# Performance work log

Measured on AMD Instinct MI355X. Metric: run time of the kernel, lower is better.

Reference implementation:

```python
import jax, jax.numpy as jnp
import numpy as np

B, T, C, H, W = 1, 8, 128, 64, 64
F = 64  # num_feat


def setup_inputs() -> dict:
    key = jax.random.key(0)
    ks = jax.random.split(key, 8)
    return {
        "input1": jax.random.normal(ks[0], (B, T, C, H, W), jnp.float32),
        "input2": jax.random.normal(ks[1], (B, T, C, H, W), jnp.float32),
        "W1": jax.random.normal(ks[2], (F, C), jnp.float32) * 0.05,
        "b1": jax.random.normal(ks[3], (F,), jnp.float32) * 0.05,
        "W2": jax.random.normal(ks[4], (F, C), jnp.float32) * 0.05,
        "b2": jax.random.normal(ks[5], (F,), jnp.float32) * 0.05,
        "W3": jax.random.normal(ks[6], (F, C), jnp.float32) * 0.05,
        "b3": jax.random.normal(ks[7], (F,), jnp.float32) * 0.05,
    }


def reference(input1, input2, W1, b1, W2, b2, W3, b3):
    # act == 0 (ReLU branch). Conv1d(kernel=1) == per-position linear projection.
    b, t, c, h, w = input1.shape
    n = h * w
    x1 = input1.reshape(b, t, c, n)  # matches transpose(1,2).reshape then frame slice
    x2 = input2.reshape(b, t, c, n)
    q = jnp.einsum('fc,btcn->btnf', W1, x1) + b1          # [B,T,N,F]
    k = jnp.einsum('fc,btcn->btnf', W2, x2) + b2          # [B,T,N,F]
    g = jnp.einsum('fc,btcn->btnf', W3, x1) + b3          # [B,T,N,F]
    scores = jax.nn.relu(jnp.einsum('btnf,btmf->btnm', q, k))  # [B,T,N,N]
    out = jnp.einsum('btnm,btmf->btnf', scores, g)        # [B,T,N,F]
    # view([B,H,W,F]).permute(0,3,1,2), stacked over T -> [B,T,F,H,W]
    return out.reshape(b, t, h, w, -1).transpose(0, 1, 4, 2, 3)
```

## Files before the change

### kernel.cpp

```cpp
#include <hip/hip_runtime.h>
#include <hip/hip_bf16.h>

constexpr int T = 8;
constexpr int C = 128;
constexpr int N = 4096;
constexpr int F = 64;

typedef __bf16 bf16x8 __attribute__((ext_vector_type(8)));
typedef __bf16 bf16x4 __attribute__((ext_vector_type(4)));
typedef __bf16 bf16x2 __attribute__((ext_vector_type(2)));
typedef float  f32x4  __attribute__((ext_vector_type(4)));
typedef float  f32x16 __attribute__((ext_vector_type(16)));

__global__ __launch_bounds__(256) void setup_kernel(
    const float* __restrict__ W1, const float* __restrict__ W2,
    const float* __restrict__ W3, __bf16* __restrict__ Wb,
    float* __restrict__ out)
{
    int i = blockIdx.x * 256 + threadIdx.x;
    ((f32x4*)out)[i] = (f32x4){0.f, 0.f, 0.f, 0.f};
    if (i < 3 * F * C) {
        int p = i >> 13, r = i & 8191;
        const float* W = (p == 0) ? W1 : (p == 1) ? W2 : W3;
        Wb[i] = (__bf16)W[r];
    }
}

__global__ __launch_bounds__(256) void proj_kernel(
    const float* __restrict__ x1, const float* __restrict__ x2,
    const __bf16* __restrict__ Wb,
    const float* __restrict__ b1, const float* __restrict__ b2,
    const float* __restrict__ b3,
    __bf16* __restrict__ Qb, __bf16* __restrict__ Kb, __bf16* __restrict__ Gw)
{
    const int pj = blockIdx.y;
    const int t  = blockIdx.x >> 6;
    const int nb = blockIdx.x & 63;
    const int n0 = nb * 64;

    constexpr int XS = 136;
    __shared__ __bf16 Xt[64 * XS];

    const float* X = (pj == 1) ? x2 : x1;

    const int tid = threadIdx.x;
    const int ng  = tid & 15;
    const int cgi = tid >> 4;

#pragma unroll
    for (int pass = 0; pass < 2; ++pass) {
        const int c0 = cgi * 4 + pass * 64;
        const size_t base = ((size_t)t * C + c0) * (size_t)N + n0 + ng * 4;
        f32x4 v[4];
#pragma unroll
        for (int i = 0; i < 4; ++i)
            v[i] = *(const f32x4*)&X[base + (size_t)i * N];
#pragma unroll
        for (int j = 0; j < 4; ++j) {
            bf16x4 o;
#pragma unroll
            for (int i = 0; i < 4; ++i) o[i] = (__bf16)v[i][j];
            *(bf16x4*)&Xt[(ng * 4 + j) * XS + c0] = o;
        }
    }
    __syncthreads();

    const int wave = tid >> 6, lane = tid & 63;
    const int quad = lane >> 4, l16 = lane & 15;

    bf16x8 a[4];
#pragma unroll
    for (int cc = 0; cc < 4; ++cc)
        a[cc] = *(const bf16x8*)&Xt[(wave * 16 + l16) * XS + cc * 32 + quad * 8];

    const __bf16* W = Wb + (size_t)pj * F * C;

    if (pj < 2) {
        const float* bias = pj ? b2 : b1;
        __bf16*      O    = pj ? Kb : Qb;

        f32x4 acc[4];
#pragma unroll
        for (int ft = 0; ft < 4; ++ft) acc[ft] = (f32x4){0.f, 0.f, 0.f, 0.f};
#pragma unroll
        for (int cc = 0; cc < 4; ++cc) {
#pragma unroll
            for (int ft = 0; ft < 4; ++ft) {
                bf16x8 wf = *(const bf16x8*)&W[(ft * 16 + l16) * C + cc * 32 + quad * 8];
                acc[ft] = __builtin_amdgcn_mfma_f32_16x16x32_bf16(wf, a[cc], acc[ft], 0, 0, 0);
            }
        }
        const int n = n0 + wave * 16 + l16;
#pragma unroll
        for (int ft = 0; ft < 4; ++ft) {
            const int f0 = ft * 16 + quad * 4;
            f32x4 bv = *(const f32x4*)&bias[f0];
            bf16x4 o;
#pragma unroll
            for (int r = 0; r < 4; ++r) o[r] = (__bf16)(acc[ft][r] + bv[r]);
            *(bf16x4*)&O[((size_t)t * N + n) * F + f0] = o;
        }
    } else {
        f32x4 acc[4];
#pragma unroll
        for (int ft = 0; ft < 4; ++ft) acc[ft] = (f32x4){0.f, 0.f, 0.f, 0.f};
#pragma unroll
        for (int cc = 0; cc < 4; ++cc) {
#pragma unroll
            for (int ft = 0; ft < 4; ++ft) {
                bf16x8 wf = *(const bf16x8*)&W[(ft * 16 + l16) * C + cc * 32 + quad * 8];
                acc[ft] = __builtin_amdgcn_mfma_f32_16x16x32_bf16(a[cc], wf, acc[ft], 0, 0, 0);
            }
        }
        const int nr0 = n0 + wave * 16 + quad * 4;
#pragma unroll
        for (int ft = 0; ft < 4; ++ft) {
            const int f = ft * 16 + l16;
            const float bv = b3[f];
            bf16x4 o;
#pragma unroll
            for (int r = 0; r < 4; ++r) o[r] = (__bf16)(acc[ft][r] + bv);
            *(bf16x4*)&Gw[((size_t)t * F + f) * (size_t)N + nr0] = o;
        }
    }
}

constexpr int KSPLIT = 4;

__global__ __launch_bounds__(512, 4) void attn_kernel(
    const __bf16* __restrict__ Qb, const __bf16* __restrict__ Kb,
    const __bf16* __restrict__ Gw, float* __restrict__ out)
{
    const int ks = blockIdx.x & (KSPLIT - 1);
    const int qb = (blockIdx.x / KSPLIT) & 15;
    const int t  = blockIdx.x / (KSPLIT * 16);
    const int q0 = qb * 256;

    constexpr int KS = 72;
    __shared__ __bf16 Kt[64 * KS];
    __shared__ __bf16 Gt[64 * KS];

    const int tid = threadIdx.x, wave = tid >> 6, lane = tid & 63;
    const int m32 = lane & 31, hi = lane >> 5;

    bf16x8 qf[4];
    {
        const __bf16* qrow = &Qb[((size_t)t * N + q0 + wave * 32 + m32) * F + hi * 8];
#pragma unroll
        for (int fc = 0; fc < 4; ++fc)
            qf[fc] = *(const bf16x8*)(qrow + fc * 16);
    }

    f32x16 oacc[2];
#pragma unroll
    for (int ft = 0; ft < 2; ++ft)
#pragma unroll
        for (int r = 0; r < 16; ++r) oacc[ft][r] = 0.f;

    const int kb_lo = ks * (N / 64 / KSPLIT);
    const int kb_hi = kb_lo + (N / 64 / KSPLIT);

    const int r8 = tid >> 3, c8 = (tid & 7) * 8;

    bf16x8 kv, gv;
    {
        const int k0 = kb_lo * 64;
        kv = *(const bf16x8*)&Kb[((size_t)t * N + k0 + r8) * F + c8];
        gv = *(const bf16x8*)&Gw[((size_t)t * F + r8) * (size_t)N + k0 + c8];
    }

    for (int kb = kb_lo; kb < kb_hi; ++kb) {
        __syncthreads();
        *(bf16x8*)&Kt[r8 * KS + c8] = kv;
        *(bf16x8*)&Gt[r8 * KS + c8] = gv;
        __syncthreads();

        if (kb + 1 < kb_hi) {
            const int k0 = (kb + 1) * 64;
            kv = *(const bf16x8*)&Kb[((size_t)t * N + k0 + r8) * F + c8];
            gv = *(const bf16x8*)&Gw[((size_t)t * F + r8) * (size_t)N + k0 + c8];
        }

        bf16x8 ps[4];
#pragma unroll
        for (int kt = 0; kt < 2; ++kt) {
            f32x16 s;
#pragma unroll
            for (int r = 0; r < 16; ++r) s[r] = 0.f;
            __builtin_amdgcn_s_setprio(1);
#pragma unroll
            for (int fc = 0; fc < 4; ++fc) {
                bf16x8 kf = *(const bf16x8*)&Kt[(kt * 32 + m32) * KS + fc * 16 + hi * 8];
                s = __builtin_amdgcn_mfma_f32_32x32x16_bf16(kf, qf[fc], s, 0, 0, 0);
            }
            __builtin_amdgcn_s_setprio(0);
            unsigned P[8];
#pragma unroll
            for (int m = 0; m < 8; ++m) {
                union { bf16x2 h; unsigned u; } pk;
                pk.h[0] = (__bf16)fmaxf(s[2 * m], 0.f);
                pk.h[1] = (__bf16)fmaxf(s[2 * m + 1], 0.f);
                P[m] = pk.u;
            }
            asm("v_permlane32_swap_b32 %0, %1" : "+v"(P[0]), "+v"(P[2]));
            asm("v_permlane32_swap_b32 %0, %1" : "+v"(P[1]), "+v"(P[3]));
            asm("v_permlane32_swap_b32 %0, %1" : "+v"(P[4]), "+v"(P[6]));
            asm("v_permlane32_swap_b32 %0, %1" : "+v"(P[5]), "+v"(P[7]));
            union { unsigned u[4]; bf16x8 v; } lo, hiu;
            lo.u[0]  = P[0]; lo.u[1]  = P[1]; lo.u[2]  = P[2]; lo.u[3]  = P[3];
            hiu.u[0] = P[4]; hiu.u[1] = P[5]; hiu.u[2] = P[6]; hiu.u[3] = P[7];
            ps[kt * 2]     = lo.v;
            ps[kt * 2 + 1] = hiu.v;
        }

        __builtin_amdgcn_s_setprio(1);
#pragma unroll
        for (int ft = 0; ft < 2; ++ft)
#pragma unroll
            for (int kt = 0; kt < 2; ++kt)
#pragma unroll
                for (int kc = 0; kc < 2; ++kc) {
                    bf16x8 gfr = *(const bf16x8*)&Gt[(ft * 32 + m32) * KS +
                                                     kt * 32 + kc * 16 + hi * 8];
                    oacc[ft] = __builtin_amdgcn_mfma_f32_32x32x16_bf16(
                        gfr, ps[kt * 2 + kc], oacc[ft], 0, 0, 0);
                }
        __builtin_amdgcn_s_setprio(0);
    }

    const int q = q0 + wave * 32 + m32;
#pragma unroll
    for (int ft = 0; ft < 2; ++ft)
#pragma unroll
        for (int r = 0; r < 16; ++r) {
            int f = ft * 32 + (r & 3) + 8 * (r >> 2) + 4 * hi;
            unsafeAtomicAdd(&out[((size_t)t * F + f) * (size_t)N + q], oacc[ft][r]);
        }
}

extern "C" void kernel_launch(void* const* d_in, const int* in_sizes, int n_in,
                              void* d_out, int out_size, void* d_ws, size_t ws_size,
                              hipStream_t stream) {
    const float* x1 = (const float*)d_in[0];
    const float* x2 = (const float*)d_in[1];
    const float* W1 = (const float*)d_in[2];
    const float* b1 = (const float*)d_in[3];
    const float* W2 = (const float*)d_in[4];
    const float* b2 = (const float*)d_in[5];
    const float* W3 = (const float*)d_in[6];
    const float* b3 = (const float*)d_in[7];
    float* out = (float*)d_out;

    __bf16* Qb = (__bf16*)d_ws;
    __bf16* Kb = Qb + (size_t)T * N * F;
    __bf16* Gw = Kb + (size_t)T * N * F;
    __bf16* Wb = Gw + (size_t)T * N * F;

    setup_kernel<<<dim3(T * F * N / 4 / 256), dim3(256), 0, stream>>>(
        W1, W2, W3, Wb, out);
    proj_kernel<<<dim3(T * (N / 64), 3), dim3(256), 0, stream>>>(
        x1, x2, Wb, b1, b2, b3, Qb, Kb, Gw);
    attn_kernel<<<dim3(T * 16 * KSPLIT), dim3(512), 0, stream>>>(Qb, Kb, Gw, out);
}
```

Before: 151.9 us.

## Fuse setup, projection and attention into one cooperative persistent kernel

Adds a fused kernel launched cooperatively with 512 blocks of 512 threads. It zeroes the output, converts the weights, then runs the Q/K/G projections, with each block loading both x1 and x2 tiles into shared memory that is unioned with the attention staging buffers. It then runs the split-K attention phase, with grid-wide syncs separating the three stages. This removes two kernel launches and their gaps, at the cost of grid barriers and a dependence on cooperative launch support. The old three-kernel path remains as a fallback.

Measured after the change: 153.2 us. No clear change (+0.9%).

```diff
diff --git a/kernel.cpp b/kernel.cpp
--- a/kernel.cpp
+++ b/kernel.cpp
@@ -1,5 +1,8 @@
 #include <hip/hip_runtime.h>
 #include <hip/hip_bf16.h>
+#include <hip/hip_cooperative_groups.h>
+
+namespace cg = cooperative_groups;
 
 constexpr int T = 8;
 constexpr int C = 128;
@@ -11,6 +14,275 @@
 typedef __bf16 bf16x2 __attribute__((ext_vector_type(2)));
 typedef float  f32x4  __attribute__((ext_vector_type(4)));
 typedef float  f32x16 __attribute__((ext_vector_type(16)));
+
+constexpr int KSPLIT = 4;
+constexpr int XS = 136;
+constexpr int KS = 72;
+
+union SMem {
+    struct { __bf16 Xt[64 * XS]; } x;
+    struct { __bf16 Kt[64 * KS]; __bf16 Gt[64 * KS]; } a;
+};
+
+__global__ __launch_bounds__(512, 4) void fused_kernel(
+    const float* __restrict__ x1, const float* __restrict__ x2,
+    const float* __restrict__ W1, const float* __restrict__ W2,
+    const float* __restrict__ W3,
+    const float* __restrict__ b1, const float* __restrict__ b2,
+    const float* __restrict__ b3,
+    __bf16* __restrict__ Qb, __bf16* __restrict__ Kb, __bf16* __restrict__ Gw,
+    __bf16* __restrict__ Wb, float* __restrict__ out)
+{
+    __shared__ SMem sm;
+    const int tid = threadIdx.x;
+    const int bid = blockIdx.x;
+
+    {
+        f32x4* o4 = (f32x4*)out;
+        const int base = bid * 1024 + tid;
+        o4[base]       = (f32x4){0.f, 0.f, 0.f, 0.f};
+        o4[base + 512] = (f32x4){0.f, 0.f, 0.f, 0.f};
+
+        int i = bid * 512 + tid;
+        if (i < 3 * F * C) {
+            int p = i >> 13, r = i & 8191;
+            const float* W = (p == 0) ? W1 : (p == 1) ? W2 : W3;
+            Wb[i] = (__bf16)W[r];
+        }
+    }
+    cg::this_grid().sync();
+
+    {
+        const int t  = bid >> 6;
+        const int nb = bid & 63;
+        const int n0 = nb * 64;
+        const int wave = tid >> 6, lane = tid & 63;
+        const int quad = lane >> 4, l16 = lane & 15;
+        const int ng = tid & 15;
+        const int c0 = (tid >> 4) * 4;
+        const int rg = wave & 3;
+
+        {
+            const size_t base = ((size_t)t * C + c0) * (size_t)N + n0 + ng * 4;
+            f32x4 v[4];
+#pragma unroll
+            for (int i = 0; i < 4; ++i) v[i] = *(const f32x4*)&x1[base + (size_t)i * N];
+#pragma unroll
+            for (int j = 0; j < 4; ++j) {
+                bf16x4 o;
+#pragma unroll
+                for (int i = 0; i < 4; ++i) o[i] = (__bf16)v[i][j];
+                *(bf16x4*)&sm.x.Xt[(ng * 4 + j) * XS + c0] = o;
+            }
+        }
+        __syncthreads();
+
+        bf16x8 a[4];
+        if (wave < 4) {
+#pragma unroll
+            for (int cc = 0; cc < 4; ++cc)
+                a[cc] = *(const bf16x8*)&sm.x.Xt[(rg * 16 + l16) * XS + cc * 32 + quad * 8];
+        }
+        __syncthreads();
+
+        {
+            const size_t base = ((size_t)t * C + c0) * (size_t)N + n0 + ng * 4;
+            f32x4 v[4];
+#pragma unroll
+            for (int i = 0; i < 4; ++i) v[i] = *(const f32x4*)&x2[base + (size_t)i * N];
+#pragma unroll
+            for (int j = 0; j < 4; ++j) {
+                bf16x4 o;
+#pragma unroll
+                for (int i = 0; i < 4; ++i) o[i] = (__bf16)v[i][j];
+                *(bf16x4*)&sm.x.Xt[(ng * 4 + j) * XS + c0] = o;
+            }
+        }
+        __syncthreads();
+
+        if (wave >= 4) {
+#pragma unroll
+            for (int cc = 0; cc < 4; ++cc)
+                a[cc] = *(const bf16x8*)&sm.x.Xt[(rg * 16 + l16) * XS + cc * 32 + quad * 8];
+        }
+
+        if (wave < 4) {
+            {
+                const __bf16* W = Wb;
+                f32x4 acc[4];
+#pragma unroll
+                for (int ft = 0; ft < 4; ++ft) acc[ft] = (f32x4){0.f, 0.f, 0.f, 0.f};
+#pragma unroll
+                for (int cc = 0; cc < 4; ++cc)
+#pragma unroll
+                    for (int ft = 0; ft < 4; ++ft) {
+                        bf16x8 wf = *(const bf16x8*)&W[(ft * 16 + l16) * C + cc * 32 + quad * 8];
+                        acc[ft] = __builtin_amdgcn_mfma_f32_16x16x32_bf16(wf, a[cc], acc[ft], 0, 0, 0);
+                    }
+                const int n = n0 + rg * 16 + l16;
+#pragma unroll
+                for (int ft = 0; ft < 4; ++ft) {
+                    const int f0 = ft * 16 + quad * 4;
+                    f32x4 bv = *(const f32x4*)&b1[f0];
+                    bf16x4 o;
+#pragma unroll
+                    for (int r = 0; r < 4; ++r) o[r] = (__bf16)(acc[ft][r] + bv[r]);
+                    *(bf16x4*)&Qb[((size_t)t * N + n) * F + f0] = o;
+                }
+            }
+            {
+                const __bf16* W = Wb + (size_t)2 * F * C;
+                f32x4 acc[4];
+#pragma unroll
+                for (int ft = 0; ft < 4; ++ft) acc[ft] = (f32x4){0.f, 0.f, 0.f, 0.f};
+#pragma unroll
+                for (int cc = 0; cc < 4; ++cc)
+#pragma unroll
+                    for (int ft = 0; ft < 4; ++ft) {
+                        bf16x8 wf = *(const bf16x8*)&W[(ft * 16 + l16) * C + cc * 32 + quad * 8];
+                        acc[ft] = __builtin_amdgcn_mfma_f32_16x16x32_bf16(a[cc], wf, acc[ft], 0, 0, 0);
+                    }
+                const int nr0 = n0 + rg * 16 + quad * 4;
+#pragma unroll
+                for (int ft = 0; ft < 4; ++ft) {
+                    const int f = ft * 16 + l16;
+                    const float bv = b3[f];
+                    bf16x4 o;
+#pragma unroll
+                    for (int r = 0; r < 4; ++r) o[r] = (__bf16)(acc[ft][r] + bv);
+                    *(bf16x4*)&Gw[((size_t)t * F + f) * (size_t)N + nr0] = o;
+                }
+            }
+        } else {
+            const __bf16* W = Wb + (size_t)F * C;
+            f32x4 acc[4];
+#pragma unroll
+            for (int ft = 0; ft < 4; ++ft) acc[ft] = (f32x4){0.f, 0.f, 0.f, 0.f};
+#pragma unroll
+            for (int cc = 0; cc < 4; ++cc)
+#pragma unroll
+                for (int ft = 0; ft < 4; ++ft) {
+                    bf16x8 wf = *(const bf16x8*)&W[(ft * 16 + l16) * C + cc * 32 + quad * 8];
+                    acc[ft] = __builtin_amdgcn_mfma_f32_16x16x32_bf16(wf, a[cc], acc[ft], 0, 0, 0);
+                }
+            const int n = n0 + rg * 16 + l16;
+#pragma unroll
+            for (int ft = 0; ft < 4; ++ft) {
+                const int f0 = ft * 16 + quad * 4;
+                f32x4 bv = *(const f32x4*)&b2[f0];
+                bf16x4 o;
+#pragma unroll
+                for (int r = 0; r < 4; ++r) o[r] = (__bf16)(acc[ft][r] + bv[r]);
+                *(bf16x4*)&Kb[((size_t)t * N + n) * F + f0] = o;
+            }
+        }
+    }
+    cg::this_grid().sync();
+
+    {
+        const int ks = bid & (KSPLIT - 1);
+        const int qb = (bid / KSPLIT) & 15;
+        const int t  = bid / (KSPLIT * 16);
+        const int q0 = qb * 256;
+
+        const int wave = tid >> 6, lane = tid & 63;
+        const int m32 = lane & 31, hi = lane >> 5;
+
+        bf16x8 qf[4];
+        {
+            const __bf16* qrow = &Qb[((size_t)t * N + q0 + wave * 32 + m32) * F + hi * 8];
+#pragma unroll
+            for (int fc = 0; fc < 4; ++fc)
+                qf[fc] = *(const bf16x8*)(qrow + fc * 16);
+        }
+
+        f32x16 oacc[2];
+#pragma unroll
+        for (int ft = 0; ft < 2; ++ft)
+#pragma unroll
+            for (int r = 0; r < 16; ++r) oacc[ft][r] = 0.f;
+
+        const int kb_lo = ks * (N / 64 / KSPLIT);
+        const int kb_hi = kb_lo + (N / 64 / KSPLIT);
+
+        const int r8 = tid >> 3, c8 = (tid & 7) * 8;
+
+        bf16x8 kv, gv;
+        {
+            const int k0 = kb_lo * 64;
+            kv = *(const bf16x8*)&Kb[((size_t)t * N + k0 + r8) * F + c8];
+            gv = *(const bf16x8*)&Gw[((size_t)t * F + r8) * (size_t)N + k0 + c8];
+        }
+
+        for (int kb = kb_lo; kb < kb_hi; ++kb) {
+            __syncthreads();
+            *(bf16x8*)&sm.a.Kt[r8 * KS + c8] = kv;
+            *(bf16x8*)&sm.a.Gt[r8 * KS + c8] = gv;
+            __syncthreads();
+
+            if (kb + 1 < kb_hi) {
+                const int k0 = (kb + 1) * 64;
+                kv = *(const bf16x8*)&Kb[((size_t)t * N + k0 + r8) * F + c8];
+                gv = *(const bf16x8*)&Gw[((size_t)t * F + r8) * (size_t)N + k0 + c8];
+            }
+
+            bf16x8 ps[4];
+#pragma unroll
+            for (int kt = 0; kt < 2; ++kt) {
+                f32x16 s;
+#pragma unroll
+                for (int r = 0; r < 16; ++r) s[r] = 0.f;
+                __builtin_amdgcn_s_setprio(1);
+#pragma unroll
+                for (int fc = 0; fc < 4; ++fc) {
+                    bf16x8 kf = *(const bf16x8*)&sm.a.Kt[(kt * 32 + m32) * KS + fc * 16 + hi * 8];
+                    s = __builtin_amdgcn_mfma_f32_32x32x16_bf16(kf, qf[fc], s, 0, 0, 0);
+                }
+                __builtin_amdgcn_s_setprio(0);
+                unsigned P[8];
+#pragma unroll
+                for (int m = 0; m < 8; ++m) {
+                    union { bf16x2 h; unsigned u; } pk;
+                    pk.h[0] = (__bf16)fmaxf(s[2 * m], 0.f);
+                    pk.h[1] = (__bf16)fmaxf(s[2 * m + 1], 0.f);
+                    P[m] = pk.u;
+                }
+                asm("v_permlane32_swap_b32 %0, %1" : "+v"(P[0]), "+v"(P[2]));
+                asm("v_permlane32_swap_b32 %0, %1" : "+v"(P[1]), "+v"(P[3]));
+                asm("v_permlane32_swap_b32 %0, %1" : "+v"(P[4]), "+v"(P[6]));
+                asm("v_permlane32_swap_b32 %0, %1" : "+v"(P[5]), "+v"(P[7]));
+                union { unsigned u[4]; bf16x8 v; } lo, hiu;
+                lo.u[0]  = P[0]; lo.u[1]  = P[1]; lo.u[2]  = P[2]; lo.u[3]  = P[3];
+                hiu.u[0] = P[4]; hiu.u[1] = P[5]; hiu.u[2] = P[6]; hiu.u[3] = P[7];
+                ps[kt * 2]     = lo.v;
+                ps[kt * 2 + 1] = hiu.v;
+            }
+
+            __builtin_amdgcn_s_setprio(1);
+#pragma unroll
+            for (int ft = 0; ft < 2; ++ft)
+#pragma unroll
+                for (int kt = 0; kt < 2; ++kt)
+#pragma unroll
+                    for (int kc = 0; kc < 2; ++kc) {
+                        bf16x8 gfr = *(const bf16x8*)&sm.a.Gt[(ft * 32 + m32) * KS +
+                                                              kt * 32 + kc * 16 + hi * 8];
+                        oacc[ft] = __builtin_amdgcn_mfma_f32_32x32x16_bf16(
+                            gfr, ps[kt * 2 + kc], oacc[ft], 0, 0, 0);
+                    }
+            __builtin_amdgcn_s_setprio(0);
+        }
+
+        const int q = q0 + wave * 32 + m32;
+#pragma unroll
+        for (int ft = 0; ft < 2; ++ft)
+#pragma unroll
+            for (int r = 0; r < 16; ++r) {
+                int f = ft * 32 + (r & 3) + 8 * (r >> 2) + 4 * hi;
+                unsafeAtomicAdd(&out[((size_t)t * F + f) * (size_t)N + q], oacc[ft][r]);
+            }
+    }
+}
 
 __global__ __launch_bounds__(256) void setup_kernel(
     const float* __restrict__ W1, const float* __restrict__ W2,
@@ -38,9 +310,7 @@
     const int nb = blockIdx.x & 63;
     const int n0 = nb * 64;
 
-    constexpr int XS = 136;
     __shared__ __bf16 Xt[64 * XS];
-
     const float* X = (pj == 1) ? x2 : x1;
 
     const int tid = threadIdx.x;
@@ -53,8 +323,7 @@
         const size_t base = ((size_t)t * C + c0) * (size_t)N + n0 + ng * 4;
         f32x4 v[4];
 #pragma unroll
-        for (int i = 0; i < 4; ++i)
-            v[i] = *(const f32x4*)&X[base + (size_t)i * N];
+        for (int i = 0; i < 4; ++i) v[i] = *(const f32x4*)&X[base + (size_t)i * N];
 #pragma unroll
         for (int j = 0; j < 4; ++j) {
             bf16x4 o;
@@ -78,18 +347,16 @@
     if (pj < 2) {
         const float* bias = pj ? b2 : b1;
         __bf16*      O    = pj ? Kb : Qb;
-
         f32x4 acc[4];
 #pragma unroll
         for (int ft = 0; ft < 4; ++ft) acc[ft] = (f32x4){0.f, 0.f, 0.f, 0.f};
 #pragma unroll
-        for (int cc = 0; cc < 4; ++cc) {
+        for (int cc = 0; cc < 4; ++cc)
 #pragma unroll
             for (int ft = 0; ft < 4; ++ft) {
                 bf16x8 wf = *(const bf16x8*)&W[(ft * 16 + l16) * C + cc * 32 + quad * 8];
                 acc[ft] = __builtin_amdgcn_mfma_f32_16x16x32_bf16(wf, a[cc], acc[ft], 0, 0, 0);
             }
-        }
         const int n = n0 + wave * 16 + l16;
 #pragma unroll
         for (int ft = 0; ft < 4; ++ft) {
@@ -105,13 +372,12 @@
 #pragma unroll
         for (int ft = 0; ft < 4; ++ft) acc[ft] = (f32x4){0.f, 0.f, 0.f, 0.f};
 #pragma unroll
-        for (int cc = 0; cc < 4; ++cc) {
+        for (int cc = 0; cc < 4; ++cc)
 #pragma unroll
             for (int ft = 0; ft < 4; ++ft) {
                 bf16x8 wf = *(const bf16x8*)&W[(ft * 16 + l16) * C + cc * 32 + quad * 8];
                 acc[ft] = __builtin_amdgcn_mfma_f32_16x16x32_bf16(a[cc], wf, acc[ft], 0, 0, 0);
             }
-        }
         const int nr0 = n0 + wave * 16 + quad * 4;
 #pragma unroll
         for (int ft = 0; ft < 4; ++ft) {
@@ -124,8 +390,6 @@
         }
     }
 }
-
-constexpr int KSPLIT = 4;
 
 __global__ __launch_bounds__(512, 4) void attn_kernel(
     const __bf16* __restrict__ Qb, const __bf16* __restrict__ Kb,
@@ -136,7 +400,6 @@
     const int t  = blockIdx.x / (KSPLIT * 16);
     const int q0 = qb * 256;
 
-    constexpr int KS = 72;
     __shared__ __bf16 Kt[64 * KS];
     __shared__ __bf16 Gt[64 * KS];
 
@@ -256,6 +519,26 @@
     __bf16* Gw = Kb + (size_t)T * N * F;
     __bf16* Wb = Gw + (size_t)T * N * F;
 
+    static int coop_ok = -1;
+    hipStreamCaptureStatus cap = hipStreamCaptureStatusNone;
+    (void)hipStreamIsCapturing(stream, &cap);
+    const bool capturing = (cap != hipStreamCaptureStatusNone);
+    const bool attempt = capturing ? (coop_ok == 1) : (coop_ok != 0);
+
+    if (attempt) {
+        void* args[] = {&x1, &x2, &W1, &W2, &W3, &b1, &b2, &b3,
+                        &Qb, &Kb, &Gw, &Wb, &out};
+        hipError_t e = hipLaunchCooperativeKernel((void*)fused_kernel,
+                                                  dim3(512), dim3(512),
+                                                  args, 0, stream);
+        if (e == hipSuccess) {
+            if (!capturing) coop_ok = 1;
+            return;
+        }
+        (void)hipGetLastError();
+        if (!capturing) coop_ok = 0;
+    }
+
     setup_kernel<<<dim3(T * F * N / 4 / 256), dim3(256), 0, stream>>>(
         W1, W2, W3, Wb, out);
     proj_kernel<<<dim3(T * (N / 64), 3), dim3(256), 0, stream>>>(
```

## Load K/G fragments directly from global into registers, drop LDS staging in attention

Applied to the files above, without the earlier changes.

The attention kernel no longer stages K and G tiles through shared memory with two barriers per iteration. Each wave now loads its MFMA operand fragments straight from global memory into registers and double-buffers them, prefetching the next tile after use. Blocks shrink to 256 threads covering 128 queries, the grid is reordered so t varies fastest, and output zeroing moves from the setup kernel into the projection kernel. This removes LDS traffic and synchronization, at the cost of redundant global/L2 reads of K and G across waves and higher register pressure.

Result: slower. 227.2 us (+49.6%).

```diff
diff --git a/kernel.cpp b/kernel.cpp
--- a/kernel.cpp
+++ b/kernel.cpp
@@ -12,18 +12,17 @@
 typedef float  f32x4  __attribute__((ext_vector_type(4)));
 typedef float  f32x16 __attribute__((ext_vector_type(16)));
 
+constexpr int KSPLIT = 4;
+constexpr int XS = 136;
+
 __global__ __launch_bounds__(256) void setup_kernel(
     const float* __restrict__ W1, const float* __restrict__ W2,
-    const float* __restrict__ W3, __bf16* __restrict__ Wb,
-    float* __restrict__ out)
+    const float* __restrict__ W3, __bf16* __restrict__ Wb)
 {
     int i = blockIdx.x * 256 + threadIdx.x;
-    ((f32x4*)out)[i] = (f32x4){0.f, 0.f, 0.f, 0.f};
-    if (i < 3 * F * C) {
-        int p = i >> 13, r = i & 8191;
-        const float* W = (p == 0) ? W1 : (p == 1) ? W2 : W3;
-        Wb[i] = (__bf16)W[r];
-    }
+    int p = i >> 13, r = i & 8191;
+    const float* W = (p == 0) ? W1 : (p == 1) ? W2 : W3;
+    Wb[i] = (__bf16)W[r];
 }
 
 __global__ __launch_bounds__(256) void proj_kernel(
@@ -31,19 +30,27 @@
     const __bf16* __restrict__ Wb,
     const float* __restrict__ b1, const float* __restrict__ b2,
     const float* __restrict__ b3,
-    __bf16* __restrict__ Qb, __bf16* __restrict__ Kb, __bf16* __restrict__ Gw)
+    __bf16* __restrict__ Qb, __bf16* __restrict__ Kb, __bf16* __restrict__ Gw,
+    float* __restrict__ out)
 {
     const int pj = blockIdx.y;
     const int t  = blockIdx.x >> 6;
     const int nb = blockIdx.x & 63;
     const int n0 = nb * 64;
 
-    constexpr int XS = 136;
     __shared__ __bf16 Xt[64 * XS];
-
     const float* X = (pj == 1) ? x2 : x1;
 
     const int tid = threadIdx.x;
+
+    if (pj == 0) {
+        f32x4* o4 = (f32x4*)out;
+        const int b0 = blockIdx.x * 1024 + tid;
+#pragma unroll
+        for (int k = 0; k < 4; ++k)
+            o4[b0 + k * 256] = (f32x4){0.f, 0.f, 0.f, 0.f};
+    }
+
     const int ng  = tid & 15;
     const int cgi = tid >> 4;
 
@@ -53,8 +60,7 @@
         const size_t base = ((size_t)t * C + c0) * (size_t)N + n0 + ng * 4;
         f32x4 v[4];
 #pragma unroll
-        for (int i = 0; i < 4; ++i)
-            v[i] = *(const f32x4*)&X[base + (size_t)i * N];
+        for (int i = 0; i < 4; ++i) v[i] = *(const f32x4*)&X[base + (size_t)i * N];
 #pragma unroll
         for (int j = 0; j < 4; ++j) {
             bf16x4 o;
@@ -78,18 +84,16 @@
     if (pj < 2) {
         const float* bias = pj ? b2 : b1;
         __bf16*      O    = pj ? Kb : Qb;
-
         f32x4 acc[4];
 #pragma unroll
         for (int ft = 0; ft < 4; ++ft) acc[ft] = (f32x4){0.f, 0.f, 0.f, 0.f};
 #pragma unroll
-        for (int cc = 0; cc < 4; ++cc) {
+        for (int cc = 0; cc < 4; ++cc)
 #pragma unroll
             for (int ft = 0; ft < 4; ++ft) {
                 bf16x8 wf = *(const bf16x8*)&W[(ft * 16 + l16) * C + cc * 32 + quad * 8];
                 acc[ft] = __builtin_amdgcn_mfma_f32_16x16x32_bf16(wf, a[cc], acc[ft], 0, 0, 0);
             }
-        }
         const int n = n0 + wave * 16 + l16;
 #pragma unroll
         for (int ft = 0; ft < 4; ++ft) {
@@ -105,13 +109,12 @@
 #pragma unroll
         for (int ft = 0; ft < 4; ++ft) acc[ft] = (f32x4){0.f, 0.f, 0.f, 0.f};
 #pragma unroll
-        for (int cc = 0; cc < 4; ++cc) {
+        for (int cc = 0; cc < 4; ++cc)
 #pragma unroll
             for (int ft = 0; ft < 4; ++ft) {
                 bf16x8 wf = *(const bf16x8*)&W[(ft * 16 + l16) * C + cc * 32 + quad * 8];
                 acc[ft] = __builtin_amdgcn_mfma_f32_16x16x32_bf16(a[cc], wf, acc[ft], 0, 0, 0);
             }
-        }
         const int nr0 = n0 + wave * 16 + quad * 4;
 #pragma unroll
         for (int ft = 0; ft < 4; ++ft) {
@@ -125,20 +128,16 @@
     }
 }
 
-constexpr int KSPLIT = 4;
-
-__global__ __launch_bounds__(512, 4) void attn_kernel(
+__global__ __launch_bounds__(256, 3) void attn_kernel(
     const __bf16* __restrict__ Qb, const __bf16* __restrict__ Kb,
     const __bf16* __restrict__ Gw, float* __restrict__ out)
 {
-    const int ks = blockIdx.x & (KSPLIT - 1);
-    const int qb = (blockIdx.x / KSPLIT) & 15;
-    const int t  = blockIdx.x / (KSPLIT * 16);
-    const int q0 = qb * 256;
-
-    constexpr int KS = 72;
-    __shared__ __bf16 Kt[64 * KS];
-    __shared__ __bf16 Gt[64 * KS];
+    const int bid = blockIdx.x;
+    const int t   = bid & 7;
+    const int rr  = bid >> 3;
+    const int ks  = rr & (KSPLIT - 1);
+    const int qb  = rr >> 2;
+    const int q0  = qb * 128;
 
     const int tid = threadIdx.x, wave = tid >> 6, lane = tid & 63;
     const int m32 = lane & 31, hi = lane >> 5;
@@ -157,29 +156,28 @@
 #pragma unroll
         for (int r = 0; r < 16; ++r) oacc[ft][r] = 0.f;
 
-    const int kb_lo = ks * (N / 64 / KSPLIT);
-    const int kb_hi = kb_lo + (N / 64 / KSPLIT);
-
-    const int r8 = tid >> 3, c8 = (tid & 7) * 8;
-
-    bf16x8 kv, gv;
+    const int kb_lo = ks * 16, kb_hi = kb_lo + 16;
+
+    const __bf16* kbase = &Kb[((size_t)t * N + m32) * F + hi * 8];
+    const __bf16* gbase = &Gw[((size_t)t * F + m32) * (size_t)N + hi * 8];
+
+    bf16x8 kf[2][4], gf[2][4];
     {
         const int k0 = kb_lo * 64;
-        kv = *(const bf16x8*)&Kb[((size_t)t * N + k0 + r8) * F + c8];
-        gv = *(const bf16x8*)&Gw[((size_t)t * F + r8) * (size_t)N + k0 + c8];
+#pragma unroll
+        for (int kt = 0; kt < 2; ++kt)
+#pragma unroll
+            for (int fc = 0; fc < 4; ++fc)
+                kf[kt][fc] = *(const bf16x8*)(kbase + (size_t)(k0 + kt * 32) * F + fc * 16);
+#pragma unroll
+        for (int ft = 0; ft < 2; ++ft)
+#pragma unroll
+            for (int kc = 0; kc < 4; ++kc)
+                gf[ft][kc] = *(const bf16x8*)(gbase + (size_t)ft * 32 * N + k0 + kc * 16);
     }
 
     for (int kb = kb_lo; kb < kb_hi; ++kb) {
-        __syncthreads();
-        *(bf16x8*)&Kt[r8 * KS + c8] = kv;
-        *(bf16x8*)&Gt[r8 * KS + c8] = gv;
-        __syncthreads();
-
-        if (kb + 1 < kb_hi) {
-            const int k0 = (kb + 1) * 64;
-            kv = *(const bf16x8*)&Kb[((size_t)t * N + k0 + r8) * F + c8];
-            gv = *(const bf16x8*)&Gw[((size_t)t * F + r8) * (size_t)N + k0 + c8];
-        }
+        const int k1 = (kb + 1 < kb_hi ? kb + 1 : kb_lo) * 64;
 
         bf16x8 ps[4];
 #pragma unroll
@@ -189,10 +187,8 @@
             for (int r = 0; r < 16; ++r) s[r] = 0.f;
             __builtin_amdgcn_s_setprio(1);
 #pragma unroll
-            for (int fc = 0; fc < 4; ++fc) {
-                bf16x8 kf = *(const bf16x8*)&Kt[(kt * 32 + m32) * KS + fc * 16 + hi * 8];
-                s = __builtin_amdgcn_mfma_f32_32x32x16_bf16(kf, qf[fc], s, 0, 0, 0);
-            }
+            for (int fc = 0; fc < 4; ++fc)
+                s = __builtin_amdgcn_mfma_f32_32x32x16_bf16(kf[kt][fc], qf[fc], s, 0, 0, 0);
             __builtin_amdgcn_s_setprio(0);
             unsigned P[8];
 #pragma unroll
@@ -213,19 +209,26 @@
             ps[kt * 2 + 1] = hiu.v;
         }
 
+#pragma unroll
+        for (int kt = 0; kt < 2; ++kt)
+#pragma unroll
+            for (int fc = 0; fc < 4; ++fc)
+                kf[kt][fc] = *(const bf16x8*)(kbase + (size_t)(k1 + kt * 32) * F + fc * 16);
+
         __builtin_amdgcn_s_setprio(1);
 #pragma unroll
         for (int ft = 0; ft < 2; ++ft)
 #pragma unroll
-            for (int kt = 0; kt < 2; ++kt)
-#pragma unroll
-                for (int kc = 0; kc < 2; ++kc) {
-                    bf16x8 gfr = *(const bf16x8*)&Gt[(ft * 32 + m32) * KS +
-                                                     kt * 32 + kc * 16 + hi * 8];
-                    oacc[ft] = __builtin_amdgcn_mfma_f32_32x32x16_bf16(
-                        gfr, ps[kt * 2 + kc], oacc[ft], 0, 0, 0);
-                }
+            for (int kc = 0; kc < 4; ++kc)
+                oacc[ft] = __builtin_amdgcn_mfma_f32_32x32x16_bf16(
+                    gf[ft][kc], ps[kc], oacc[ft], 0, 0, 0);
         __builtin_amdgcn_s_setprio(0);
+
+#pragma unroll
+        for (int ft = 0; ft < 2; ++ft)
+#pragma unroll
+            for (int kc = 0; kc < 4; ++kc)
+                gf[ft][kc] = *(const bf16x8*)(gbase + (size_t)ft * 32 * N + k1 + kc * 16);
     }
 
     const int q = q0 + wave * 32 + m32;
@@ -256,9 +259,8 @@
     __bf16* Gw = Kb + (size_t)T * N * F;
     __bf16* Wb = Gw + (size_t)T * N * F;
 
-    setup_kernel<<<dim3(T * F * N / 4 / 256), dim3(256), 0, stream>>>(
-        W1, W2, W3, Wb, out);
+    setup_kernel<<<dim3(3 * F * C / 256), dim3(256), 0, stream>>>(W1, W2, W3, Wb);
     proj_kernel<<<dim3(T * (N / 64), 3), dim3(256), 0, stream>>>(
-        x1, x2, Wb, b1, b2, b3, Qb, Kb, Gw);
-    attn_kernel<<<dim3(T * 16 * KSPLIT), dim3(512), 0, stream>>>(Qb, Kb, Gw, out);
-}
+        x1, x2, Wb, b1, b2, b3, Qb, Kb, Gw, out);
+    attn_kernel<<<dim3(T * KSPLIT * 32), dim3(256), 0, stream>>>(Qb, Kb, Gw, out);
+}
```
